# Kernel optimization log

Hardware: AMD Instinct MI355X
Metric: run time of the kernel (lower is better)

Reference implementation:

```python
import jax, jax.numpy as jnp
import numpy as np

DIM = 192
HEADS = 8
B = 8
HH = 128
WW = 128
EPS_BN = 1e-5
EPS_NORM = 1e-12


def _bn(x, g, b, m, v):
    # inference-mode BatchNorm2d over channel axis 1, x: (B,C,H,W)
    inv = g / jnp.sqrt(v + EPS_BN)
    return x * inv[None, :, None, None] + (b - m * inv)[None, :, None, None]


def _gelu(x):
    return jax.nn.gelu(x, approximate=False)


def setup_inputs() -> dict:
    key = jax.random.key(0)
    ks = jax.random.split(key, 16)
    d, h8, h16 = DIM, DIM // 8, DIM // 16
    N = HH * WW
    s = 0.02
    inp = {
        "x": jax.random.normal(ks[0], (B, N, d), jnp.float32),
        "H": HH,
        "W": WW,
        "w_qkv": jax.random.normal(ks[1], (d, 3 * d), jnp.float32) * s,
        "temperature": jnp.ones((HEADS, 1, 1), jnp.float32),
        "dw_w": jax.random.normal(ks[2], (d, 1, 3, 3), jnp.float32) * s,
        "dw_b": jnp.zeros((d,), jnp.float32),
        "bn1_g": jnp.ones((d,), jnp.float32), "bn1_b": jnp.zeros((d,), jnp.float32),
        "bn1_m": jnp.zeros((d,), jnp.float32), "bn1_v": jnp.ones((d,), jnp.float32),
        "ci_w1": jax.random.normal(ks[3], (h8, d), jnp.float32) * s,
        "ci_b1": jnp.zeros((h8,), jnp.float32),
        "bn2_g": jnp.ones((h8,), jnp.float32), "bn2_b": jnp.zeros((h8,), jnp.float32),
        "bn2_m": jnp.zeros((h8,), jnp.float32), "bn2_v": jnp.ones((h8,), jnp.float32),
        "ci_w2": jax.random.normal(ks[4], (d, h8), jnp.float32) * s,
        "ci_b2": jnp.zeros((d,), jnp.float32),
        "si_w1": jax.random.normal(ks[5], (h16, d), jnp.float32) * s,
        "si_b1": jnp.zeros((h16,), jnp.float32),
        "bn3_g": jnp.ones((h16,), jnp.float32), "bn3_b": jnp.zeros((h16,), jnp.float32),
        "bn3_m": jnp.zeros((h16,), jnp.float32), "bn3_v": jnp.ones((h16,), jnp.float32),
        "si_w2": jax.random.normal(ks[6], (1, h16), jnp.float32) * s,
        "si_b2": jnp.zeros((1,), jnp.float32),
        "proj_w": jax.random.normal(ks[7], (d, d), jnp.float32) * s,
        "proj_b": jnp.zeros((d,), jnp.float32),
    }
    return inp


def reference(x, H, W, w_qkv, temperature, dw_w, dw_b,
              bn1_g, bn1_b, bn1_m, bn1_v,
              ci_w1, ci_b1, bn2_g, bn2_b, bn2_m, bn2_v, ci_w2, ci_b2,
              si_w1, si_b1, bn3_g, bn3_b, bn3_m, bn3_v, si_w2, si_b2,
              proj_w, proj_b):
    Bn, N, C = x.shape
    hd = C // HEADS
    # qkv projection (no bias), split into heads: (3,B,h,N,hd)
    qkv = (x @ w_qkv).reshape(Bn, N, 3, HEADS, hd).transpose(2, 0, 3, 1, 4)
    q = qkv[0].transpose(0, 1, 3, 2)  # (B,h,hd,N)
    k = qkv[1].transpose(0, 1, 3, 2)
    v = qkv[2].transpose(0, 1, 3, 2)
    v_img = v.reshape(Bn, C, N).reshape(Bn, C, H, W)
    # L2-normalize along token axis (F.normalize eps=1e-12)
    q = q / jnp.clip(jnp.linalg.norm(q, axis=-1, keepdims=True), EPS_NORM)
    k = k / jnp.clip(jnp.linalg.norm(k, axis=-1, keepdims=True), EPS_NORM)
    attn = jnp.einsum('bhcn,bhdn->bhcd', q, k) * temperature  # (B,h,hd,hd)
    attn = jax.nn.softmax(attn, axis=-1)
    att_x = jnp.einsum('bhcd,bhdn->bhcn', attn, v)  # (B,h,hd,N)
    att_x = att_x.transpose(0, 3, 1, 2).reshape(Bn, N, C)
    # depthwise conv branch: 3x3 dw conv + BN + GELU
    conv_x = jax.lax.conv_general_dilated(
        v_img, dw_w, window_strides=(1, 1), padding='SAME',
        dimension_numbers=('NCHW', 'OIHW', 'NCHW'), feature_group_count=C)
    conv_x = _gelu(_bn(conv_x + dw_b[None, :, None, None], bn1_g, bn1_b, bn1_m, bn1_v))
    # channel interaction: SE gate computed from attention branch
    att_img = att_x.transpose(0, 2, 1).reshape(Bn, C, H, W)
    pooled = jnp.mean(att_img, axis=(2, 3), keepdims=True)  # (B,C,1,1)
    cm = jnp.einsum('bcij,oc->boij', pooled, ci_w1) + ci_b1[None, :, None, None]
    cm = _gelu(_bn(cm, bn2_g, bn2_b, bn2_m, bn2_v))
    channel_map = jnp.einsum('bcij,oc->boij', cm, ci_w2) + ci_b2[None, :, None, None]
    # spatial interaction: gate computed from conv branch
    sm = jnp.einsum('bchw,oc->bohw', conv_x, si_w1) + si_b1[None, :, None, None]
    sm = _gelu(_bn(sm, bn3_g, bn3_b, bn3_m, bn3_v))
    spatial_map = jnp.einsum('bchw,oc->bohw', sm, si_w2) + si_b2[None, :, None, None]
    spatial_map = spatial_map.transpose(0, 2, 3, 1).reshape(Bn, N, 1)
    # cross gating
    att_x = att_x * jax.nn.sigmoid(spatial_map)
    conv_x = conv_x * jax.nn.sigmoid(channel_map)
    conv_x = conv_x.transpose(0, 2, 3, 1).reshape(Bn, N, C)
    out = (att_x + conv_x) @ proj_w + proj_b
    return out
```

## Files before the change

### kernel.cpp

```cpp
#include <hip/hip_runtime.h>
#include <math.h>

#define Bb 8
#define Cc 192
#define NHEADS 8
#define HDim 24
#define Him 128
#define Wim 128
#define Ntok 16384
#define EPSBN 1e-5f

typedef __bf16 bf16x8 __attribute__((ext_vector_type(8)));
typedef __bf16 bf16x2 __attribute__((ext_vector_type(2)));
typedef float  f32x4  __attribute__((ext_vector_type(4)));

static __device__ __forceinline__ float gelu_f(float v) {
    return 0.5f * v * (1.0f + erff(v * 0.70710678118654752f));
}
static __device__ __forceinline__ float sigmoid_f(float v) {
    return 1.0f / (1.0f + expf(-v));
}
static __device__ __forceinline__ void split8(const float* xv, bf16x8& h8, bf16x8& l8) {
#pragma unroll
    for (int j = 0; j < 8; ++j) {
        float v = xv[j];
        __bf16 h = (__bf16)v;
        h8[j] = h;
        l8[j] = (__bf16)(v - (float)h);
    }
}

__global__ __launch_bounds__(256) void k_wprep(const float* __restrict__ w,
                                               __bf16* __restrict__ wt)
{
    int idx = blockIdx.x * 256 + threadIdx.x;
    if (idx >= 36864) return;
    int k = idx / 192, c = idx % 192;
    float v = w[k * 576 + 384 + c];
    __bf16 h = (__bf16)v;
    __bf16 l = (__bf16)(v - (float)h);
    wt[c * 192 + k] = h;
    wt[36864 + c * 192 + k] = l;
}

__global__ __launch_bounds__(256, 2) void k_xtx(const float* __restrict__ x,
                                                float* __restrict__ xpart)
{
    __shared__ __align__(16) __bf16 Th[192 * 40];
    __shared__ __align__(16) __bf16 Tl[192 * 40];
    const int t = threadIdx.x;
    const int lane = t & 63, wave = t >> 6;
    const int chunk = blockIdx.x;
    const int b = blockIdx.y;
    const int n0 = chunk * 512;
    const int m16 = lane & 15, q = lane >> 4;
    const int rq = (wave & 1) * 6;
    const int cq = (wave >> 1) * 6;

    f32x4 acc[6][6];
#pragma unroll
    for (int i = 0; i < 6; ++i)
#pragma unroll
        for (int j = 0; j < 6; ++j)
#pragma unroll
            for (int r = 0; r < 4; ++r) acc[i][j][r] = 0.f;

    int u0 = t, u1 = t + 256, u2 = t + 512;
    const int ch4_0 = (u0 % 48) * 4, tk_0 = (u0 / 48) * 2;
    const int ch4_1 = (u1 % 48) * 4, tk_1 = (u1 / 48) * 2;
    const int ch4_2 = (u2 % 48) * 4, tk_2 = (u2 / 48) * 2;
    const float* xb = x + ((size_t)b * Ntok + n0) * 192;
    const float* p0 = xb + (size_t)tk_0 * 192 + ch4_0;
    const float* p1 = xb + (size_t)tk_1 * 192 + ch4_1;
    const float* p2 = xb + (size_t)tk_2 * 192 + ch4_2;
    const int o0 = ch4_0 * 40 + tk_0;
    const int o1 = ch4_1 * 40 + tk_1;
    const int o2 = ch4_2 * 40 + tk_2;

    for (int ks = 0; ks < 16; ++ks) {
        __syncthreads();
        {
            const float* pp[3] = { p0, p1, p2 };
            const int oo[3] = { o0, o1, o2 };
#pragma unroll
            for (int j = 0; j < 3; ++j) {
                const float* p = pp[j] + (size_t)ks * 32 * 192;
                float4 a = *(const float4*)p;
                float4 c = *(const float4*)(p + 192);
#pragma unroll
                for (int cix = 0; cix < 4; ++cix) {
                    float v0 = (&a.x)[cix], v1 = (&c.x)[cix];
                    __bf16 h0 = (__bf16)v0, h1 = (__bf16)v1;
                    __bf16 l0 = (__bf16)(v0 - (float)h0);
                    __bf16 l1 = (__bf16)(v1 - (float)h1);
                    int o = oo[j] + cix * 40;
                    bf16x2 hp; hp[0] = h0; hp[1] = h1;
                    bf16x2 lp; lp[0] = l0; lp[1] = l1;
                    *(bf16x2*)&Th[o] = hp;
                    *(bf16x2*)&Tl[o] = lp;
                }
            }
        }
        __syncthreads();

#pragma unroll
        for (int rb = 0; rb < 2; ++rb) {
            bf16x8 fah[3], fal[3];
#pragma unroll
            for (int g = 0; g < 3; ++g) {
                int o = ((rq + rb * 3 + g) * 16 + m16) * 40 + q * 8;
                fah[g] = *(const bf16x8*)&Th[o];
                fal[g] = *(const bf16x8*)&Tl[o];
            }
#pragma unroll
            for (int cb = 0; cb < 2; ++cb) {
                bf16x8 fbh[3], fbl[3];
#pragma unroll
                for (int g = 0; g < 3; ++g) {
                    int o = ((cq + cb * 3 + g) * 16 + m16) * 40 + q * 8;
                    fbh[g] = *(const bf16x8*)&Th[o];
                    fbl[g] = *(const bf16x8*)&Tl[o];
                }
#pragma unroll
                for (int ti = 0; ti < 3; ++ti)
#pragma unroll
                    for (int tj = 0; tj < 3; ++tj) {
                        f32x4& a = acc[rb * 3 + ti][cb * 3 + tj];
                        a = __builtin_amdgcn_mfma_f32_16x16x32_bf16(fah[ti], fbh[tj], a, 0, 0, 0);
                        a = __builtin_amdgcn_mfma_f32_16x16x32_bf16(fah[ti], fbl[tj], a, 0, 0, 0);
                        a = __builtin_amdgcn_mfma_f32_16x16x32_bf16(fal[ti], fbh[tj], a, 0, 0, 0);
                    }
            }
        }
    }
    float* op = xpart + ((size_t)b * 32 + chunk) * 36864;
#pragma unroll
    for (int ti = 0; ti < 6; ++ti)
#pragma unroll
        for (int tj = 0; tj < 6; ++tj) {
            const int row0 = (rq + ti) * 16 + q * 4;
            const int col = (cq + tj) * 16 + m16;
#pragma unroll
            for (int j = 0; j < 4; ++j)
                op[(size_t)(row0 + j) * 192 + col] = acc[ti][tj][j];
        }
}

__global__ __launch_bounds__(256) void k_xred(const float* __restrict__ xpart,
                                              float* __restrict__ XtX)
{
    const int b = blockIdx.y;
    const int e = blockIdx.x * 256 + threadIdx.x;
    const float* p = xpart + (size_t)b * 32 * 36864 + e;
    float s = 0.f;
#pragma unroll
    for (int c = 0; c < 32; ++c) s += p[(size_t)c * 36864];
    XtX[(size_t)b * 36864 + e] = s;
}

__global__ __launch_bounds__(256) void k_gram2(const float* __restrict__ XtX,
                                               const float* __restrict__ w_qkv,
                                               float* __restrict__ gram,
                                               float* __restrict__ ssq_q,
                                               float* __restrict__ ssq_k)
{
    __shared__ float wq[192][24];
    __shared__ float wk[192][24];
    __shared__ float U[192][24];
    __shared__ float V[192][24];
    const int b = blockIdx.x, h = blockIdx.y, t = threadIdx.x;
    for (int e = t; e < 4608; e += 256) {
        int k = e / 24, c = e % 24;
        wq[k][c] = w_qkv[k * 576 + h * 24 + c];
        wk[k][c] = w_qkv[k * 576 + 192 + h * 24 + c];
    }
    __syncthreads();
    if (t < 192) {
        const float* xr = XtX + (size_t)b * 36864 + (size_t)t * 192;
        float u[24], v[24];
#pragma unroll
        for (int c = 0; c < 24; ++c) { u[c] = 0.f; v[c] = 0.f; }
        for (int k4 = 0; k4 < 48; ++k4) {
            float4 x4 = *(const float4*)(xr + k4 * 4);
#pragma unroll
            for (int kk = 0; kk < 4; ++kk) {
                float xv = (&x4.x)[kk];
                int k = k4 * 4 + kk;
#pragma unroll
                for (int c = 0; c < 24; ++c) {
                    u[c] = fmaf(xv, wq[k][c], u[c]);
                    v[c] = fmaf(xv, wk[k][c], v[c]);
                }
            }
        }
#pragma unroll
        for (int c = 0; c < 24; ++c) { U[t][c] = u[c]; V[t][c] = v[c]; }
    }
    __syncthreads();
    for (int o = t; o < 576; o += 256) {
        int c = o / 24, d = o % 24;
        float g = 0.f;
        for (int r = 0; r < 192; ++r) g = fmaf(wq[r][c], V[r][d], g);
        gram[(size_t)(b * NHEADS + h) * 576 + o] = g;
    }
    if (t < 24) {
        float s = 0.f;
        for (int r = 0; r < 192; ++r) s = fmaf(wq[r][t], U[r][t], s);
        ssq_q[b * Cc + h * HDim + t] = s;
    } else if (t < 48) {
        int c = t - 24;
        float s = 0.f;
        for (int r = 0; r < 192; ++r) s = fmaf(wk[r][c], V[r][c], s);
        ssq_k[b * Cc + h * HDim + c] = s;
    }
}

__global__ __launch_bounds__(256, 2) void k_qkv_mfma(const float* __restrict__ x,
                                                     const __bf16* __restrict__ wt,
                                                     float* __restrict__ vout,
                                                     float* __restrict__ vsum)
{
    __shared__ __align__(16) __bf16 Ah[128 * 40];
    __shared__ __align__(16) __bf16 Al[128 * 40];
    __shared__ __align__(16) __bf16 Bh[192 * 40];
    __shared__ __align__(16) __bf16 Bl[192 * 40];

    const int t = threadIdx.x;
    const int lane = t & 63, wave = t >> 6;
    const int n0 = blockIdx.x * 128;
    const int b = blockIdx.y;
    const int row_base = (wave & 1) * 64;
    const int col_base = (wave >> 1) * 96;
    const int m16 = lane & 15, q = lane >> 4;

    f32x4 acc[4][6];
#pragma unroll
    for (int rt = 0; rt < 4; ++rt)
#pragma unroll
        for (int ct = 0; ct < 6; ++ct)
#pragma unroll
            for (int j = 0; j < 4; ++j) acc[rt][ct][j] = 0.f;

    const int ar = t >> 1, ahalf = t & 1;
    const float* xrow = x + ((size_t)b * Ntok + n0 + ar) * Cc + ahalf * 16;

    for (int kc = 0; kc < 6; ++kc) {
        {
            const float4* xp4 = (const float4*)(xrow + kc * 32);
            float xv[16];
            float4 u;
            u = xp4[0]; xv[0] = u.x; xv[1] = u.y; xv[2]  = u.z; xv[3]  = u.w;
            u = xp4[1]; xv[4] = u.x; xv[5] = u.y; xv[6]  = u.z; xv[7]  = u.w;
            u = xp4[2]; xv[8] = u.x; xv[9] = u.y; xv[10] = u.z; xv[11] = u.w;
            u = xp4[3]; xv[12] = u.x; xv[13] = u.y; xv[14] = u.z; xv[15] = u.w;
            bf16x8 vh0, vh1, vl0, vl1;
            split8(xv, vh0, vl0);
            split8(xv + 8, vh1, vl1);
            const int o = ar * 40 + ahalf * 16;
            *(bf16x8*)&Ah[o] = vh0; *(bf16x8*)&Ah[o + 8] = vh1;
            *(bf16x8*)&Al[o] = vl0; *(bf16x8*)&Al[o + 8] = vl1;
        }
#pragma unroll
        for (int i = 0; i < 3; ++i) {
            int f = i * 256 + t;
            int n = f >> 2, k8 = (f & 3) << 3;
            const __bf16* src = wt + (size_t)n * 192 + kc * 32 + k8;
            bf16x8 vh = *(const bf16x8*)src;
            bf16x8 vl = *(const bf16x8*)(src + 36864);
            *(bf16x8*)&Bh[n * 40 + k8] = vh;
            *(bf16x8*)&Bl[n * 40 + k8] = vl;
        }
        __syncthreads();

        bf16x8 fah[4], fal[4], fbh[6], fbl[6];
#pragma unroll
        for (int rt = 0; rt < 4; ++rt) {
            int o = (row_base + rt * 16 + m16) * 40 + q * 8;
            fah[rt] = *(const bf16x8*)&Ah[o];
            fal[rt] = *(const bf16x8*)&Al[o];
        }
#pragma unroll
        for (int ct = 0; ct < 6; ++ct) {
            int o = (col_base + ct * 16 + m16) * 40 + q * 8;
            fbh[ct] = *(const bf16x8*)&Bh[o];
            fbl[ct] = *(const bf16x8*)&Bl[o];
        }
#pragma unroll
        for (int rt = 0; rt < 4; ++rt)
#pragma unroll
            for (int ct = 0; ct < 6; ++ct) {
                acc[rt][ct] = __builtin_amdgcn_mfma_f32_16x16x32_bf16(
                    fah[rt], fbh[ct], acc[rt][ct], 0, 0, 0);
                acc[rt][ct] = __builtin_amdgcn_mfma_f32_16x16x32_bf16(
                    fah[rt], fbl[ct], acc[rt][ct], 0, 0, 0);
                acc[rt][ct] = __builtin_amdgcn_mfma_f32_16x16x32_bf16(
                    fal[rt], fbh[ct], acc[rt][ct], 0, 0, 0);
            }
        __syncthreads();
    }

    const size_t obase = (size_t)b * Cc * (size_t)Ntok;
#pragma unroll
    for (int rt = 0; rt < 4; ++rt)
#pragma unroll
        for (int ct = 0; ct < 6; ++ct) {
            int token = n0 + row_base + rt * 16 + q * 4;
            int col = col_base + ct * 16 + m16;
            float4 o = make_float4(acc[rt][ct][0], acc[rt][ct][1],
                                   acc[rt][ct][2], acc[rt][ct][3]);
            *(float4*)(vout + obase + (size_t)col * Ntok + token) = o;
        }

#pragma unroll
    for (int ct = 0; ct < 6; ++ct) {
        float s = 0.f;
#pragma unroll
        for (int rt = 0; rt < 4; ++rt)
            s += acc[rt][ct][0] + acc[rt][ct][1] + acc[rt][ct][2] + acc[rt][ct][3];
        s += __shfl_xor(s, 16, 64);
        s += __shfl_xor(s, 32, 64);
        if (q == 0)
            atomicAdd(vsum + b * Cc + col_base + ct * 16 + m16, s);
    }
}

__global__ __launch_bounds__(256) void k_attn(const float* __restrict__ gram,
                                              const float* __restrict__ ssq_q,
                                              const float* __restrict__ ssq_k,
                                              const float* __restrict__ temperature,
                                              const float* __restrict__ vmean,
                                              const float* __restrict__ ci_w1,
                                              const float* __restrict__ ci_b1,
                                              const float* __restrict__ bn2_g,
                                              const float* __restrict__ bn2_b,
                                              const float* __restrict__ bn2_m,
                                              const float* __restrict__ bn2_v,
                                              const float* __restrict__ ci_w2,
                                              const float* __restrict__ ci_b2,
                                              float* __restrict__ attn,
                                              float* __restrict__ sig_ch)
{
    __shared__ float pooled[192];
    __shared__ float cmv[24];
    const int b = blockIdx.x, t = threadIdx.x;
    if (t < 192) {
        int h = t / 24, c = t % 24;
        const float* gp = gram + (size_t)(b * NHEADS + h) * 576 + c * 24;
        float qn = fmaxf(sqrtf(ssq_q[b * Cc + h * HDim + c]), 1e-12f);
        float temp = temperature[h];
        float logit[24];
        float m = -1e30f;
#pragma unroll
        for (int d = 0; d < 24; ++d) {
            float kn = fmaxf(sqrtf(ssq_k[b * Cc + h * HDim + d]), 1e-12f);
            float l = gp[d] / (qn * kn) * temp;
            logit[d] = l; m = fmaxf(m, l);
        }
        float s = 0.f;
#pragma unroll
        for (int d = 0; d < 24; ++d) { float e = expf(logit[d] - m); logit[d] = e; s += e; }
        float inv = 1.f / s;
        float pool = 0.f;
        float* ap = attn + (size_t)(b * NHEADS + h) * 576 + c * 24;
#pragma unroll
        for (int d = 0; d < 24; ++d) {
            float a = logit[d] * inv;
            ap[d] = a;
            pool = fmaf(a, vmean[b * Cc + h * HDim + d], pool);
        }
        pooled[h * 24 + c] = pool * (1.0f / (float)Ntok);
    }
    __syncthreads();
    if (t < 24) {
        float z = ci_b1[t];
        for (int c = 0; c < 192; ++c) z = fmaf(ci_w1[t * 192 + c], pooled[c], z);
        float sc = bn2_g[t] / sqrtf(bn2_v[t] + EPSBN);
        z = z * sc + (bn2_b[t] - bn2_m[t] * sc);
        cmv[t] = gelu_f(z);
    }
    __syncthreads();
    if (t < 192) {
        float z = ci_b2[t];
#pragma unroll
        for (int o = 0; o < 24; ++o) z = fmaf(ci_w2[t * 24 + o], cmv[o], z);
        sig_ch[b * Cc + t] = sigmoid_f(z);
    }
}

__global__ __launch_bounds__(192) void k_pprep(const float* __restrict__ attn,
                                               const float* __restrict__ sig_ch,
                                               const float* __restrict__ proj_w,
                                               __bf16* __restrict__ Pt)
{
    const int b = blockIdx.x, part = blockIdx.y, j = threadIdx.x;
    __bf16* base = Pt + (size_t)b * (2 * 73728);
    if (part < 8) {
        const int h = part;
        __shared__ float at[576];
        for (int e = j; e < 576; e += 192) at[e] = attn[(size_t)(b * 8 + h) * 576 + e];
        __syncthreads();
        float pr[24];
#pragma unroll
        for (int cl = 0; cl < 24; ++cl) pr[cl] = proj_w[(h * 24 + cl) * 192 + j];
        float s[24];
#pragma unroll
        for (int d = 0; d < 24; ++d) s[d] = 0.f;
#pragma unroll
        for (int cl = 0; cl < 24; ++cl) {
            float a = pr[cl];
#pragma unroll
            for (int d = 0; d < 24; ++d) s[d] = fmaf(a, at[cl * 24 + d], s[d]);
        }
#pragma unroll
        for (int d = 0; d < 24; ++d) {
            float v = s[d];
            __bf16 hi = (__bf16)v;
            base[j * 384 + h * 24 + d] = hi;
            base[73728 + j * 384 + h * 24 + d] = (__bf16)(v - (float)hi);
        }
    } else {
        __shared__ float sch_s[192];
        sch_s[j] = sig_ch[b * Cc + j];
        __syncthreads();
        for (int ch = 0; ch < 192; ++ch) {
            float v = sch_s[ch] * proj_w[ch * 192 + j];
            __bf16 hi = (__bf16)v;
            base[j * 384 + 192 + ch] = hi;
            base[73728 + j * 384 + 192 + ch] = (__bf16)(v - (float)hi);
        }
    }
}

__global__ __launch_bounds__(256) void k_conv(const float* __restrict__ vbuf,
                                              const float* __restrict__ dw_w,
                                              const float* __restrict__ dw_b,
                                              const float* __restrict__ bn1_g,
                                              const float* __restrict__ bn1_b,
                                              const float* __restrict__ bn1_m,
                                              const float* __restrict__ bn1_v,
                                              float* __restrict__ convx)
{
    __shared__ float dww[72];
    __shared__ float scl[8], shf[8];
    const int t = threadIdx.x;
    const int y0 = blockIdx.x * 8;
    const int ch0 = blockIdx.y * 8;
    const int b = blockIdx.z;

    if (t < 72) {
        dww[t] = dw_w[ch0 * 9 + t];
    } else if (t < 80) {
        int c = t - 72, ch = ch0 + c;
        float sc = bn1_g[ch] / sqrtf(bn1_v[ch] + EPSBN);
        scl[c] = sc;
        shf[c] = (dw_b[ch] - bn1_m[ch]) * sc + bn1_b[ch];
    }
    __syncthreads();

    const int xq = (t & 31) * 4;
    const int r = t >> 5;
    const int gy = y0 + r;

#pragma unroll
    for (int ch = 0; ch < 8; ++ch) {
        const float* base = vbuf + ((size_t)b * Cc + ch0 + ch) * Ntok;
        float v[3][6];
#pragma unroll
        for (int dy = 0; dy < 3; ++dy) {
            int iy = gy - 1 + dy;
            if (iy >= 0 && iy < Him) {
                const float* rp = base + (size_t)iy * Wim;
                float4 m = *(const float4*)(rp + xq);
                v[dy][1] = m.x; v[dy][2] = m.y; v[dy][3] = m.z; v[dy][4] = m.w;
                v[dy][0] = (xq > 0) ? rp[xq - 1] : 0.f;
                v[dy][5] = (xq < 124) ? rp[xq + 4] : 0.f;
            } else {
#pragma unroll
                for (int i2 = 0; i2 < 6; ++i2) v[dy][i2] = 0.f;
            }
        }
        const float w0 = dww[ch * 9 + 0], w1 = dww[ch * 9 + 1], w2 = dww[ch * 9 + 2];
        const float w3 = dww[ch * 9 + 3], w4 = dww[ch * 9 + 4], w5 = dww[ch * 9 + 5];
        const float w6 = dww[ch * 9 + 6], w7 = dww[ch * 9 + 7], w8 = dww[ch * 9 + 8];
        const float sc = scl[ch], sh = shf[ch];
        float4 o;
#pragma unroll
        for (int p = 0; p < 4; ++p) {
            float s = v[0][p] * w0 + v[0][p + 1] * w1 + v[0][p + 2] * w2
                    + v[1][p] * w3 + v[1][p + 1] * w4 + v[1][p + 2] * w5
                    + v[2][p] * w6 + v[2][p + 1] * w7 + v[2][p + 2] * w8;
            (&o.x)[p] = gelu_f(s * sc + sh);
        }
        *(float4*)(convx + ((size_t)b * Cc + ch0 + ch) * Ntok
                   + (size_t)gy * Wim + xq) = o;
    }
}

__global__ __launch_bounds__(256, 2) void k_final_mfma(const float* __restrict__ vbuf,
                                                       const float* __restrict__ convx,
                                                       const __bf16* __restrict__ Pt,
                                                       const float* __restrict__ si_w1,
                                                       const float* __restrict__ si_b1,
                                                       const float* __restrict__ bn3_g,
                                                       const float* __restrict__ bn3_b,
                                                       const float* __restrict__ bn3_m,
                                                       const float* __restrict__ bn3_v,
                                                       const float* __restrict__ si_w2,
                                                       const float* __restrict__ si_b2,
                                                       const float* __restrict__ proj_b,
                                                       float* __restrict__ out)
{
    __shared__ __align__(16) __bf16 Ah[128 * 40];
    __shared__ __align__(16) __bf16 Al[128 * 40];
    __shared__ __align__(16) __bf16 Bh[192 * 40];
    __shared__ __align__(16) __bf16 Bl[192 * 40];
    __shared__ float smbuf[128][17];
    __shared__ float ssp_s[128];

    const int t = threadIdx.x;
    const int lane = t & 63, wave = t >> 6;
    const int n0 = blockIdx.x * 128;
    const int b = blockIdx.y;
    const int row_base = (wave & 1) * 64;
    const int col_base = (wave >> 1) * 96;
    const int m16 = lane & 15, q = lane >> 4;

    const int an = t & 127;
    const int akh = (t >> 7) & 1;
    const __bf16* ptb = Pt + (size_t)b * (2 * 73728);

    f32x4 acc[4][6];
#pragma unroll
    for (int rt = 0; rt < 4; ++rt)
#pragma unroll
        for (int ct = 0; ct < 6; ++ct)
#pragma unroll
            for (int j = 0; j < 4; ++j) acc[rt][ct][j] = 0.f;
    f32x4 accS[4];
#pragma unroll
    for (int rt = 0; rt < 4; ++rt)
#pragma unroll
        for (int j = 0; j < 4; ++j) accS[rt][j] = 0.f;

    for (int phase = 0; phase < 2; ++phase) {
        if (phase == 1) {
#pragma unroll
            for (int rt = 0; rt < 4; ++rt) {
                int row = row_base + rt * 16 + q * 4;
#pragma unroll
                for (int j = 0; j < 4; ++j)
                    smbuf[row + j][m16] = accS[rt][j];
            }
            __syncthreads();
            if (t < 128) {
                float sp = si_b2[0];
#pragma unroll
                for (int o = 0; o < 12; ++o) {
                    float z = smbuf[t][o] + si_b1[o];
                    float sc = bn3_g[o] / sqrtf(bn3_v[o] + EPSBN);
                    z = z * sc + (bn3_b[o] - bn3_m[o] * sc);
                    sp = fmaf(si_w2[o], gelu_f(z), sp);
                }
                ssp_s[t] = sigmoid_f(sp);
            }
            __syncthreads();
        }
        for (int ki = 0; ki < 6; ++ki) {
            const int kc = (phase == 0) ? (ki + 6) : ki;
            {
                const int ch0 = ki * 32 + akh * 16;
                const float* src;
                float scale;
                if (phase == 0) {
                    src = convx + ((size_t)b * Cc + ch0) * Ntok + n0 + an;
                    scale = 1.f;
                } else {
                    src = vbuf + ((size_t)b * Cc + ch0) * Ntok + n0 + an;
                    scale = ssp_s[an];
                }
                float xv[16];
#pragma unroll
                for (int jj = 0; jj < 16; ++jj)
                    xv[jj] = src[(size_t)jj * Ntok] * scale;
                bf16x8 vh0, vl0, vh1, vl1;
                split8(xv, vh0, vl0);
                split8(xv + 8, vh1, vl1);
                const int o = an * 40 + akh * 16;
                *(bf16x8*)&Ah[o] = vh0; *(bf16x8*)&Ah[o + 8] = vh1;
                *(bf16x8*)&Al[o] = vl0; *(bf16x8*)&Al[o + 8] = vl1;
            }
#pragma unroll
            for (int i = 0; i < 3; ++i) {
                int f = i * 256 + t;
                int col = f >> 2, k8 = (f & 3) << 3;
                const __bf16* sp = ptb + (size_t)col * 384 + kc * 32 + k8;
                bf16x8 vh = *(const bf16x8*)sp;
                bf16x8 vl = *(const bf16x8*)(sp + 73728);
                *(bf16x8*)&Bh[col * 40 + k8] = vh;
                *(bf16x8*)&Bl[col * 40 + k8] = vl;
            }
            __syncthreads();

            bf16x8 fah[4], fal[4], fbh[6], fbl[6];
#pragma unroll
            for (int rt = 0; rt < 4; ++rt) {
                int o = (row_base + rt * 16 + m16) * 40 + q * 8;
                fah[rt] = *(const bf16x8*)&Ah[o];
                fal[rt] = *(const bf16x8*)&Al[o];
            }
#pragma unroll
            for (int ct = 0; ct < 6; ++ct) {
                int o = (col_base + ct * 16 + m16) * 40 + q * 8;
                fbh[ct] = *(const bf16x8*)&Bh[o];
            }
#pragma unroll
            for (int rt = 0; rt < 4; ++rt)
#pragma unroll
                for (int ct = 0; ct < 6; ++ct) {
                    acc[rt][ct] = __builtin_amdgcn_mfma_f32_16x16x32_bf16(
                        fah[rt], fbh[ct], acc[rt][ct], 0, 0, 0);
                    acc[rt][ct] = __builtin_amdgcn_mfma_f32_16x16x32_bf16(
                        fal[rt], fbh[ct], acc[rt][ct], 0, 0, 0);
                }
#pragma unroll
            for (int ct = 0; ct < 6; ++ct) {
                int o = (col_base + ct * 16 + m16) * 40 + q * 8;
                fbl[ct] = *(const bf16x8*)&Bl[o];
            }
#pragma unroll
            for (int rt = 0; rt < 4; ++rt)
#pragma unroll
                for (int ct = 0; ct < 6; ++ct)
                    acc[rt][ct] = __builtin_amdgcn_mfma_f32_16x16x32_bf16(
                        fah[rt], fbl[ct], acc[rt][ct], 0, 0, 0);

            if (phase == 0) {
                bf16x8 w1h, w1l;
                if (m16 < 12) {
                    const float* wp = si_w1 + m16 * 192 + ki * 32 + q * 8;
                    float wv[8];
                    float4 u0 = *(const float4*)wp, u1 = *(const float4*)(wp + 4);
                    wv[0] = u0.x; wv[1] = u0.y; wv[2] = u0.z; wv[3] = u0.w;
                    wv[4] = u1.x; wv[5] = u1.y; wv[6] = u1.z; wv[7] = u1.w;
                    split8(wv, w1h, w1l);
                } else {
#pragma unroll
                    for (int j = 0; j < 8; ++j) { w1h[j] = (__bf16)0.f; w1l[j] = (__bf16)0.f; }
                }
#pragma unroll
                for (int rt = 0; rt < 4; ++rt) {
                    accS[rt] = __builtin_amdgcn_mfma_f32_16x16x32_bf16(
                        fah[rt], w1h, accS[rt], 0, 0, 0);
                    accS[rt] = __builtin_amdgcn_mfma_f32_16x16x32_bf16(
                        fal[rt], w1h, accS[rt], 0, 0, 0);
                    accS[rt] = __builtin_amdgcn_mfma_f32_16x16x32_bf16(
                        fah[rt], w1l, accS[rt], 0, 0, 0);
                }
            }
            __syncthreads();
        }
    }

    float* ob = out + ((size_t)b * Ntok + n0) * Cc;
#pragma unroll
    for (int ct = 0; ct < 6; ++ct) {
        const int col = col_base + ct * 16 + m16;
        const float pbv = proj_b[col];
#pragma unroll
        for (int rt = 0; rt < 4; ++rt) {
            const int row = row_base + rt * 16 + q * 4;
#pragma unroll
            for (int j = 0; j < 4; ++j)
                ob[(size_t)(row + j) * Cc + col] = acc[rt][ct][j] + pbv;
        }
    }
}

extern "C" void kernel_launch(void* const* d_in, const int* in_sizes, int n_in,
                              void* d_out, int out_size, void* d_ws, size_t ws_size,
                              hipStream_t stream)
{
    const float* x      = (const float*)d_in[0];
    const float* w_qkv  = (const float*)d_in[3];
    const float* temperature = (const float*)d_in[4];
    const float* dw_w   = (const float*)d_in[5];
    const float* dw_b   = (const float*)d_in[6];
    const float* bn1_g  = (const float*)d_in[7];
    const float* bn1_b  = (const float*)d_in[8];
    const float* bn1_m  = (const float*)d_in[9];
    const float* bn1_v  = (const float*)d_in[10];
    const float* ci_w1  = (const float*)d_in[11];
    const float* ci_b1  = (const float*)d_in[12];
    const float* bn2_g  = (const float*)d_in[13];
    const float* bn2_b  = (const float*)d_in[14];
    const float* bn2_m  = (const float*)d_in[15];
    const float* bn2_v  = (const float*)d_in[16];
    const float* ci_w2  = (const float*)d_in[17];
    const float* ci_b2  = (const float*)d_in[18];
    const float* si_w1  = (const float*)d_in[19];
    const float* si_b1  = (const float*)d_in[20];
    const float* bn3_g  = (const float*)d_in[21];
    const float* bn3_b  = (const float*)d_in[22];
    const float* bn3_m  = (const float*)d_in[23];
    const float* bn3_v  = (const float*)d_in[24];
    const float* si_w2  = (const float*)d_in[25];
    const float* si_b2  = (const float*)d_in[26];
    const float* proj_w = (const float*)d_in[27];
    const float* proj_b = (const float*)d_in[28];

    float* ws = (float*)d_ws;
    const size_t BCN = (size_t)Bb * Cc * Ntok;
    float* vbuf  = ws;
    float* convx = ws + BCN;
    __bf16* Pt   = (__bf16*)(ws + 2 * BCN);
    float* xpart = ws + 2 * BCN + 589824;
    float* XtX   = xpart + 9437184;
    float* gram  = XtX + 294912;
    float* ssq_q = gram + 36864;
    float* ssq_k = ssq_q + 1536;
    float* vmean = ssq_k + 1536;
    float* attn  = vmean + 1536;
    float* sig_ch = attn + 36864;
    float* out = (float*)d_out;

    __bf16* wt = (__bf16*)(out + BCN - 36864);

    hipMemsetAsync(vmean, 0, 1536 * sizeof(float), stream);

    k_wprep<<<dim3(144), 256, 0, stream>>>(w_qkv, wt);
    k_xtx<<<dim3(32, Bb), 256, 0, stream>>>(x, xpart);
    k_xred<<<dim3(144, Bb), 256, 0, stream>>>(xpart, XtX);
    k_gram2<<<dim3(Bb, NHEADS), 256, 0, stream>>>(XtX, w_qkv, gram, ssq_q, ssq_k);
    k_qkv_mfma<<<dim3(Ntok / 128, Bb), 256, 0, stream>>>(x, wt, vbuf, vmean);
    k_attn<<<dim3(Bb), 256, 0, stream>>>(gram, ssq_q, ssq_k, temperature, vmean,
                                         ci_w1, ci_b1, bn2_g, bn2_b, bn2_m, bn2_v,
                                         ci_w2, ci_b2, attn, sig_ch);
    k_pprep<<<dim3(Bb, 9), 192, 0, stream>>>(attn, sig_ch, proj_w, Pt);
    k_conv<<<dim3(Him / 8, Cc / 8, Bb), 256, 0, stream>>>(
        vbuf, dw_w, dw_b, bn1_g, bn1_b, bn1_m, bn1_v, convx);
    k_final_mfma<<<dim3(Ntok / 128, Bb), 256, 0, stream>>>(
        vbuf, convx, Pt, si_w1, si_b1, bn3_g, bn3_b, bn3_m, bn3_v,
        si_w2, si_b2, proj_b, out);
}
```

Before: 559.6 us.

## Double k_xtx waves to 512 threads and swizzle LDS transpose layout

The X^T X partial kernel now launches 512 threads per block with 8 waves, each owning a 6x3 tile grid of accumulators instead of 6x6, halving per-thread accumulator registers. Global loads are redistributed so each thread loads one or two float4 pairs. The LDS layout gains an XOR-like rotation of 8-token groups by channel to reduce bank conflicts on the transposed writes and fragment reads. The aim is more latency hiding and fewer LDS conflicts, at the cost of extra A-fragment reloads per wave and more waves competing for LDS bandwidth.

```diff
diff --git a/kernel.cpp b/kernel.cpp
--- a/kernel.cpp
+++ b/kernel.cpp
@@ -43,7 +43,7 @@
     wt[36864 + c * 192 + k] = l;
 }
 
-__global__ __launch_bounds__(256, 2) void k_xtx(const float* __restrict__ x,
+__global__ __launch_bounds__(512, 2) void k_xtx(const float* __restrict__ x,
                                                 float* __restrict__ xpart)
 {
     __shared__ __align__(16) __bf16 Th[192 * 40];
@@ -55,45 +55,53 @@
     const int n0 = chunk * 512;
     const int m16 = lane & 15, q = lane >> 4;
     const int rq = (wave & 1) * 6;
-    const int cq = (wave >> 1) * 6;
-
-    f32x4 acc[6][6];
+    const int cq = (wave >> 1) * 3;
+
+    f32x4 acc[6][3];
 #pragma unroll
     for (int i = 0; i < 6; ++i)
 #pragma unroll
-        for (int j = 0; j < 6; ++j)
+        for (int j = 0; j < 3; ++j)
 #pragma unroll
             for (int r = 0; r < 4; ++r) acc[i][j][r] = 0.f;
 
-    int u0 = t, u1 = t + 256, u2 = t + 512;
-    const int ch4_0 = (u0 % 48) * 4, tk_0 = (u0 / 48) * 2;
+    const int ch4_0 = (t % 48) * 4, tk_0 = (t / 48) * 2;
+    const int u1 = 512 + t;
     const int ch4_1 = (u1 % 48) * 4, tk_1 = (u1 / 48) * 2;
-    const int ch4_2 = (u2 % 48) * 4, tk_2 = (u2 / 48) * 2;
+    const bool has2 = (t < 256);
     const float* xb = x + ((size_t)b * Ntok + n0) * 192;
-    const float* p0 = xb + (size_t)tk_0 * 192 + ch4_0;
-    const float* p1 = xb + (size_t)tk_1 * 192 + ch4_1;
-    const float* p2 = xb + (size_t)tk_2 * 192 + ch4_2;
-    const int o0 = ch4_0 * 40 + tk_0;
-    const int o1 = ch4_1 * 40 + tk_1;
-    const int o2 = ch4_2 * 40 + tk_2;
 
     for (int ks = 0; ks < 16; ++ks) {
         __syncthreads();
         {
-            const float* pp[3] = { p0, p1, p2 };
-            const int oo[3] = { o0, o1, o2 };
-#pragma unroll
-            for (int j = 0; j < 3; ++j) {
-                const float* p = pp[j] + (size_t)ks * 32 * 192;
-                float4 a = *(const float4*)p;
-                float4 c = *(const float4*)(p + 192);
+            const float* p = xb + (size_t)(ks * 32 + tk_0) * 192 + ch4_0;
+            float4 a = *(const float4*)p;
+            float4 c = *(const float4*)(p + 192);
+#pragma unroll
+            for (int cix = 0; cix < 4; ++cix) {
+                int ch = ch4_0 + cix;
+                float v0 = (&a.x)[cix], v1 = (&c.x)[cix];
+                __bf16 h0 = (__bf16)v0, h1 = (__bf16)v1;
+                __bf16 l0 = (__bf16)(v0 - (float)h0);
+                __bf16 l1 = (__bf16)(v1 - (float)h1);
+                int o = ch * 40 + ((((tk_0 >> 3) + (ch >> 3)) & 3) << 3) + (tk_0 & 7);
+                bf16x2 hp; hp[0] = h0; hp[1] = h1;
+                bf16x2 lp; lp[0] = l0; lp[1] = l1;
+                *(bf16x2*)&Th[o] = hp;
+                *(bf16x2*)&Tl[o] = lp;
+            }
+            if (has2) {
+                const float* p2 = xb + (size_t)(ks * 32 + tk_1) * 192 + ch4_1;
+                float4 a2 = *(const float4*)p2;
+                float4 c2 = *(const float4*)(p2 + 192);
 #pragma unroll
                 for (int cix = 0; cix < 4; ++cix) {
-                    float v0 = (&a.x)[cix], v1 = (&c.x)[cix];
+                    int ch = ch4_1 + cix;
+                    float v0 = (&a2.x)[cix], v1 = (&c2.x)[cix];
                     __bf16 h0 = (__bf16)v0, h1 = (__bf16)v1;
                     __bf16 l0 = (__bf16)(v0 - (float)h0);
                     __bf16 l1 = (__bf16)(v1 - (float)h1);
-                    int o = oo[j] + cix * 40;
+                    int o = ch * 40 + ((((tk_1 >> 3) + (ch >> 3)) & 3) << 3) + (tk_1 & 7);
                     bf16x2 hp; hp[0] = h0; hp[1] = h1;
                     bf16x2 lp; lp[0] = l0; lp[1] = l1;
                     *(bf16x2*)&Th[o] = hp;
@@ -103,33 +111,26 @@
         }
         __syncthreads();
 
-#pragma unroll
-        for (int rb = 0; rb < 2; ++rb) {
-            bf16x8 fah[3], fal[3];
-#pragma unroll
-            for (int g = 0; g < 3; ++g) {
-                int o = ((rq + rb * 3 + g) * 16 + m16) * 40 + q * 8;
-                fah[g] = *(const bf16x8*)&Th[o];
-                fal[g] = *(const bf16x8*)&Tl[o];
-            }
-#pragma unroll
-            for (int cb = 0; cb < 2; ++cb) {
-                bf16x8 fbh[3], fbl[3];
-#pragma unroll
-                for (int g = 0; g < 3; ++g) {
-                    int o = ((cq + cb * 3 + g) * 16 + m16) * 40 + q * 8;
-                    fbh[g] = *(const bf16x8*)&Th[o];
-                    fbl[g] = *(const bf16x8*)&Tl[o];
-                }
-#pragma unroll
-                for (int ti = 0; ti < 3; ++ti)
-#pragma unroll
-                    for (int tj = 0; tj < 3; ++tj) {
-                        f32x4& a = acc[rb * 3 + ti][cb * 3 + tj];
-                        a = __builtin_amdgcn_mfma_f32_16x16x32_bf16(fah[ti], fbh[tj], a, 0, 0, 0);
-                        a = __builtin_amdgcn_mfma_f32_16x16x32_bf16(fah[ti], fbl[tj], a, 0, 0, 0);
-                        a = __builtin_amdgcn_mfma_f32_16x16x32_bf16(fal[ti], fbh[tj], a, 0, 0, 0);
-                    }
+        bf16x8 fah[6], fal[6];
+#pragma unroll
+        for (int ti = 0; ti < 6; ++ti) {
+            int ch = (rq + ti) * 16 + m16;
+            int o = ch * 40 + (((q + (ch >> 3)) & 3) << 3);
+            fah[ti] = *(const bf16x8*)&Th[o];
+            fal[ti] = *(const bf16x8*)&Tl[o];
+        }
+#pragma unroll
+        for (int tj = 0; tj < 3; ++tj) {
+            int ch = (cq + tj) * 16 + m16;
+            int o = ch * 40 + (((q + (ch >> 3)) & 3) << 3);
+            bf16x8 fbh = *(const bf16x8*)&Th[o];
+            bf16x8 fbl = *(const bf16x8*)&Tl[o];
+#pragma unroll
+            for (int ti = 0; ti < 6; ++ti) {
+                f32x4& a = acc[ti][tj];
+                a = __builtin_amdgcn_mfma_f32_16x16x32_bf16(fah[ti], fbh, a, 0, 0, 0);
+                a = __builtin_amdgcn_mfma_f32_16x16x32_bf16(fah[ti], fbl, a, 0, 0, 0);
+                a = __builtin_amdgcn_mfma_f32_16x16x32_bf16(fal[ti], fbh, a, 0, 0, 0);
             }
         }
     }
@@ -137,7 +138,7 @@
 #pragma unroll
     for (int ti = 0; ti < 6; ++ti)
 #pragma unroll
-        for (int tj = 0; tj < 6; ++tj) {
+        for (int tj = 0; tj < 3; ++tj) {
             const int row0 = (rq + ti) * 16 + q * 4;
             const int col = (cq + tj) * 16 + m16;
 #pragma unroll
@@ -728,7 +729,7 @@
     hipMemsetAsync(vmean, 0, 1536 * sizeof(float), stream);
 
     k_wprep<<<dim3(144), 256, 0, stream>>>(w_qkv, wt);
-    k_xtx<<<dim3(32, Bb), 256, 0, stream>>>(x, xpart);
+    k_xtx<<<dim3(32, Bb), 512, 0, stream>>>(x, xpart);
     k_xred<<<dim3(144, Bb), 256, 0, stream>>>(xpart, XtX);
     k_gram2<<<dim3(Bb, NHEADS), 256, 0, stream>>>(XtX, w_qkv, gram, ssq_q, ssq_k);
     k_qkv_mfma<<<dim3(Ntok / 128, Bb), 256, 0, stream>>>(x, wt, vbuf, vmean);
```

Result: faster. 529.5 us (-5.4%).
